# Kernel optimization log

Measured on AMD Instinct MI355X. Metric: run time of the kernel, lower is better.

## Reference

```python
import jax, jax.numpy as jnp
import numpy as np

N_NODES = 50000
N_EDGES = 800000
N_HIDDEN = 64
N_LAYER = 3
IN_DIM = 4


def setup_inputs() -> dict:
    key = jax.random.key(0)
    ks = jax.random.split(key, 10)
    x = jax.random.normal(ks[0], (N_NODES, IN_DIM), dtype=jnp.float32)
    edge_index = jax.random.randint(ks[1], (2, N_EDGES), 0, N_NODES, dtype=jnp.int64)
    # Glorot-style params matching pyg GCNConv (lin has no bias; conv adds bias after aggregation)
    def glorot(k, fan_in, fan_out):
        s = jnp.sqrt(6.0 / (fan_in + fan_out))
        return jax.random.uniform(k, (fan_in, fan_out), jnp.float32, -s, s)
    W_in = glorot(ks[2], IN_DIM, N_HIDDEN)
    b_in = jnp.zeros((N_HIDDEN,), jnp.float32)
    W_h = jnp.stack([glorot(jax.random.fold_in(ks[3], i), N_HIDDEN, N_HIDDEN) for i in range(N_LAYER)])
    b_h = jnp.zeros((N_LAYER, N_HIDDEN), jnp.float32)
    W_out = glorot(ks[4], N_HIDDEN, 1)
    b_out = jnp.zeros((1,), jnp.float32)
    return {"x": x, "edge_index": edge_index, "W_in": W_in, "b_in": b_in,
            "W_h": W_h, "b_h": b_h, "W_out": W_out, "b_out": b_out}


def _gcn_norm(edge_index, n_nodes):
    # add self-loops, compute symmetric norm D^{-1/2} (A+I) D^{-1/2}
    loop = jnp.arange(n_nodes, dtype=edge_index.dtype)
    src = jnp.concatenate([edge_index[0], loop])
    dst = jnp.concatenate([edge_index[1], loop])
    deg = jax.ops.segment_sum(jnp.ones_like(dst, dtype=jnp.float32), dst, num_segments=n_nodes)
    dinv = jax.lax.rsqrt(deg)  # deg >= 1 due to self-loops
    norm = dinv[src] * dinv[dst]
    return src, dst, norm


def _gcn_conv(x, W, b, src, dst, norm, n_nodes):
    h = x @ W                                   # [N, out]
    msg = h[src] * norm[:, None]                # gather + scale, [E+N, out]
    out = jax.ops.segment_sum(msg, dst, num_segments=n_nodes)  # scatter-add
    return out + b


def reference(x, edge_index, W_in, b_in, W_h, b_h, W_out, b_out):
    n = x.shape[0]
    src, dst, norm = _gcn_norm(edge_index, n)
    h = jax.nn.relu(_gcn_conv(x, W_in, b_in, src, dst, norm, n))
    for i in range(W_h.shape[0]):
        h = jax.nn.relu(_gcn_conv(h, W_h[i], b_h[i], src, dst, norm, n))
    return _gcn_conv(h, W_out, b_out, src, dst, norm, n)
```

## Files before the change

kernel.cpp:

```cpp
#include <hip/hip_runtime.h>
#include <hip/hip_bf16.h>


#define TPB 256
#define EPT 8
#define CHUNK (TPB * EPT)
typedef __hip_bfloat16 bf16;
#define B2F __bfloat162float

__global__ void k_zero_b(int* __restrict__ bktcnt, int* __restrict__ ticket) {
    bktcnt[threadIdx.x] = 0;
    if (threadIdx.x == 0) *ticket = 0;
}

__global__ __launch_bounds__(TPB) void k_bktcnt(
    const int* __restrict__ dst, int* __restrict__ bktcnt, int* __restrict__ ticket,
    int* __restrict__ bktbase, int* __restrict__ bcur, int E, int n) {
    __shared__ int h[256];
    __shared__ int lastFlag;
    int tid = threadIdx.x;
    h[tid] = 0;
    __syncthreads();
    int e0 = blockIdx.x * CHUNK;
#pragma unroll
    for (int u = 0; u < EPT; ++u) {
        int e = e0 + u * TPB + tid;
        if (e < E) {
            int d = dst[e];
            if ((unsigned)d < (unsigned)n) atomicAdd(&h[d >> 8], 1);
        }
    }
    __syncthreads();
    if (h[tid]) atomicAdd(&bktcnt[tid], h[tid]);
    __threadfence();
    __syncthreads();
    if (tid == 0) lastFlag = (atomicAdd(ticket, 1) == (int)gridDim.x - 1);
    __syncthreads();
    if (!lastFlag) return;
    int v = atomicAdd(&bktcnt[tid], 0);
    h[tid] = v;
    __syncthreads();
    for (int off = 1; off < 256; off <<= 1) {
        int u2 = (tid >= off) ? h[tid - off] : 0;
        __syncthreads();
        h[tid] += u2;
        __syncthreads();
    }
    int excl = h[tid] - v;
    bktbase[tid] = excl;
    bcur[tid] = excl;
    if (tid == 255) bktbase[256] = h[tid];
}

__global__ __launch_bounds__(TPB) void k_bin(
    const int* __restrict__ src, const int* __restrict__ dst,
    int* __restrict__ bcur, unsigned* __restrict__ staging, int E, int n) {
    __shared__ int hcnt[256];
    __shared__ int hbase[256];
    int tid = threadIdx.x;
    int e0 = blockIdx.x * CHUNK;
    hcnt[tid] = 0;
    __syncthreads();

    int eb[EPT];
    unsigned rec[EPT];
#pragma unroll
    for (int u = 0; u < EPT; ++u) {
        int e = e0 + u * TPB + tid;
        eb[u] = -1;
        if (e < E) {
            int d = dst[e], s = src[e];
            if ((unsigned)d < (unsigned)n && (unsigned)s < (unsigned)n) {
                eb[u] = d >> 8;
                rec[u] = (unsigned)s | ((unsigned)(d & 255) << 16);
                atomicAdd(&hcnt[eb[u]], 1);
            }
        }
    }
    __syncthreads();
    int c = hcnt[tid];
    hbase[tid] = (c > 0) ? atomicAdd(&bcur[tid], c) : 0;
    hcnt[tid] = 0;
    __syncthreads();
#pragma unroll
    for (int u = 0; u < EPT; ++u) {
        if (eb[u] >= 0) {
            int r = atomicAdd(&hcnt[eb[u]], 1);
            int pos = hbase[eb[u]] + r;
            if ((unsigned)pos < (unsigned)E) staging[pos] = rec[u];
        }
    }
}

__global__ __launch_bounds__(TPB) void k_unbin2(
    const unsigned* __restrict__ staging, const int* __restrict__ bktbase,
    const float* __restrict__ x, float4* __restrict__ xt,
    int* __restrict__ row_start, float* __restrict__ dinv,
    unsigned short* __restrict__ bucket, int E, int n) {
    __shared__ int cnt[256];
    __shared__ int scn[256];
    __shared__ int cur[256];
    int b = blockIdx.x, tid = threadIdx.x;
    int lo = bktbase[b], hi = bktbase[b + 1];
    lo = max(0, min(lo, E)); hi = max(lo, min(hi, E));

    cnt[tid] = 0;
    __syncthreads();
    for (int i = lo + tid; i < hi; i += TPB)
        atomicAdd(&cnt[(staging[i] >> 16) & 255], 1);
    __syncthreads();

    int v = cnt[tid];
    scn[tid] = v;
    __syncthreads();
    for (int off = 1; off < 256; off <<= 1) {
        int u = (tid >= off) ? scn[tid - off] : 0;
        __syncthreads();
        scn[tid] += u;
        __syncthreads();
    }
    int excl = scn[tid] - v;
    int base = min(lo + excl, E);
    cur[tid] = base;
    int d = (b << 8) + tid;
    if (d < n) {
        row_start[d] = base;
        float di = rsqrtf((float)v + 1.0f);
        dinv[d] = di;
        float4 xv = ((const float4*)x)[d];
        xv.x *= di; xv.y *= di; xv.z *= di; xv.w *= di;
        xt[d] = xv;
        if (d == n - 1) row_start[n] = min(base + v, E);
    }
    __syncthreads();

    for (int i = lo + tid; i < hi; i += TPB) {
        unsigned r = staging[i];
        int t = (r >> 16) & 255;
        int pos = atomicAdd(&cur[t], 1);
        if ((unsigned)pos < (unsigned)E) bucket[pos] = (unsigned short)(r & 0xffffu);
    }
}

__device__ __forceinline__ void acc_oct(float* a, uint4 w) {
    a[0] += __uint_as_float(w.x << 16);
    a[1] += __uint_as_float(w.x & 0xffff0000u);
    a[2] += __uint_as_float(w.y << 16);
    a[3] += __uint_as_float(w.y & 0xffff0000u);
    a[4] += __uint_as_float(w.z << 16);
    a[5] += __uint_as_float(w.z & 0xffff0000u);
    a[6] += __uint_as_float(w.w << 16);
    a[7] += __uint_as_float(w.w & 0xffff0000u);
}

__device__ __forceinline__ void agg_oct(const bf16* __restrict__ g,
                                        const unsigned short* __restrict__ bucket,
                                        int k0, int k1, int d, float* __restrict__ a,
                                        int lane, unsigned nm1, unsigned Em1) {
    int grp = lane >> 3, i = lane & 7;
#pragma unroll
    for (int m = 0; m < 8; ++m) a[m] = 0.f;
    if (grp == 0) {
        uint4 w = *(const uint4*)(g + (size_t)d * 64 + 8 * i);
        acc_oct(a, w);
    }
    for (int base = k0; base < k1; base += 64) {
        int cnt = min(64, k1 - base);
        int rec = bucket[min((unsigned)(base + lane), Em1)];
        int k = 0;
        for (; k + 16 <= cnt; k += 16) {
            unsigned s0 = min((unsigned)__shfl(rec, k + grp), nm1);
            unsigned s1 = min((unsigned)__shfl(rec, k + 8 + grp), nm1);
            uint4 w0 = *(const uint4*)(g + (size_t)s0 * 64 + 8 * i);
            uint4 w1 = *(const uint4*)(g + (size_t)s1 * 64 + 8 * i);
            acc_oct(a, w0);
            acc_oct(a, w1);
        }
        for (; k < cnt; k += 8) {
            int e = k + grp;
            unsigned s = min((unsigned)__shfl(rec, min(e, 63)), nm1);
            uint4 w = *(const uint4*)(g + (size_t)s * 64 + 8 * i);
            if (e < cnt) acc_oct(a, w);
        }
    }
}

__global__ __launch_bounds__(TPB, 4) void k_gconv1(
    const float4* __restrict__ xt, const float* __restrict__ dinv,
    const int* __restrict__ row_start, const unsigned short* __restrict__ bucket,
    const float* __restrict__ W_in, const float* __restrict__ b_in,
    const float* __restrict__ Wh0, bf16* __restrict__ gOut, int n, int E) {
    __shared__ float sAct[4][64];
    int tid = threadIdx.x;
    int r = tid >> 6, j = tid & 63;
    unsigned nm1 = (unsigned)(n - 1);

    float wreg[64];
#pragma unroll
    for (int k = 0; k < 64; ++k) wreg[k] = Wh0[k * 64 + j];
    float win0 = W_in[0 * 64 + j], win1 = W_in[1 * 64 + j];
    float win2 = W_in[2 * 64 + j], win3 = W_in[3 * 64 + j];
    float bj = b_in[j];

    int nw = gridDim.x * 4;
    for (int d = blockIdx.x * 4 + r; d < n; d += nw) {
        float dd = dinv[d];
        int k0 = row_start[d], k1 = row_start[d + 1];
        k1 = min(k1, E); k0 = max(min(k0, k1), 0);

        float4 v = make_float4(0.f, 0.f, 0.f, 0.f);
        if (j == 0) v = xt[d];
        for (int k = k0 + j; k < k1; k += 64) {
            unsigned s = min((unsigned)bucket[k], nm1);
            float4 t = xt[s];
            v.x += t.x; v.y += t.y; v.z += t.z; v.w += t.w;
        }
#pragma unroll
        for (int off = 1; off < 64; off <<= 1) {
            v.x += __shfl_xor(v.x, off);
            v.y += __shfl_xor(v.y, off);
            v.z += __shfl_xor(v.z, off);
            v.w += __shfl_xor(v.w, off);
        }
        float dot = fmaf(v.x, win0, fmaf(v.y, win1, fmaf(v.z, win2, v.w * win3)));
        float act = fmaxf(fmaf(dd, dot, bj), 0.f);
        sAct[r][j] = act;

        float acc0 = 0.f, acc1 = 0.f, acc2 = 0.f, acc3 = 0.f;
        const float4* ap = (const float4*)&sAct[r][0];
#pragma unroll
        for (int k4 = 0; k4 < 16; ++k4) {
            float4 av = ap[k4];
            acc0 = fmaf(av.x, wreg[4 * k4 + 0], acc0);
            acc1 = fmaf(av.y, wreg[4 * k4 + 1], acc1);
            acc2 = fmaf(av.z, wreg[4 * k4 + 2], acc2);
            acc3 = fmaf(av.w, wreg[4 * k4 + 3], acc3);
        }
        float acc = (acc0 + acc1) + (acc2 + acc3);
        gOut[(size_t)d * 64 + j] = __float2bfloat16(acc * dd);
    }
}

__global__ __launch_bounds__(TPB, 4) void k_gconv(
    const bf16* __restrict__ gIn, const float* __restrict__ dinv,
    const int* __restrict__ row_start, const unsigned short* __restrict__ bucket,
    const float* __restrict__ bias, const float* __restrict__ W,
    bf16* __restrict__ gOut, int n, int E) {
    __shared__ float sVp[4][8][68];
    int tid = threadIdx.x;
    int r = tid >> 6, j = tid & 63;
    int grp = j >> 3, i = j & 7;
    unsigned nm1 = (unsigned)(n - 1), Em1 = (unsigned)(E - 1);

    float wreg[64];
#pragma unroll
    for (int k = 0; k < 64; ++k) wreg[k] = W[k * 64 + j];
    float bj = bias[j];

    int nw = gridDim.x * 4;
    for (int d = blockIdx.x * 4 + r; d < n; d += nw) {
        float dd = dinv[d];
        int k0 = row_start[d], k1 = row_start[d + 1];
        k1 = min(k1, E); k0 = max(min(k0, k1), 0);

        float a[8];
        agg_oct(gIn, bucket, k0, k1, d, a, j, nm1, Em1);

        float4* prow = (float4*)&sVp[r][grp][8 * i];
        prow[0] = make_float4(a[0], a[1], a[2], a[3]);
        prow[1] = make_float4(a[4], a[5], a[6], a[7]);
        float full = 0.f;
#pragma unroll
        for (int g = 0; g < 8; ++g) full += sVp[r][g][j];

        float act = fmaxf(fmaf(dd, full, bj), 0.f);
        sVp[r][0][j] = act;

        float acc0 = 0.f, acc1 = 0.f, acc2 = 0.f, acc3 = 0.f;
#pragma unroll
        for (int k4 = 0; k4 < 16; ++k4) {
            float4 av = *(const float4*)&sVp[r][0][4 * k4];
            acc0 = fmaf(av.x, wreg[4 * k4 + 0], acc0);
            acc1 = fmaf(av.y, wreg[4 * k4 + 1], acc1);
            acc2 = fmaf(av.z, wreg[4 * k4 + 2], acc2);
            acc3 = fmaf(av.w, wreg[4 * k4 + 3], acc3);
        }
        float acc = (acc0 + acc1) + (acc2 + acc3);
        gOut[(size_t)d * 64 + j] = __float2bfloat16(acc * dd);
    }
}

__global__ __launch_bounds__(TPB) void k_gconv_z(
    const bf16* __restrict__ gIn, const float* __restrict__ dinv,
    const int* __restrict__ row_start, const unsigned short* __restrict__ bucket,
    const float* __restrict__ bias, const float* __restrict__ Wout,
    float* __restrict__ zg, int n, int E) {
    __shared__ float sVp[4][8][68];
    int tid = threadIdx.x;
    int r = tid >> 6, j = tid & 63;
    int grp = j >> 3, i = j & 7;
    int d = blockIdx.x * 4 + r;
    if (d >= n) return;
    float dd = dinv[d];
    int k0 = row_start[d], k1 = row_start[d + 1];
    k1 = min(k1, E); k0 = max(min(k0, k1), 0);

    float a[8];
    agg_oct(gIn, bucket, k0, k1, d, a, j, (unsigned)(n - 1), (unsigned)(E - 1));

    float4* prow = (float4*)&sVp[r][grp][8 * i];
    prow[0] = make_float4(a[0], a[1], a[2], a[3]);
    prow[1] = make_float4(a[4], a[5], a[6], a[7]);
    float full = 0.f;
#pragma unroll
    for (int g = 0; g < 8; ++g) full += sVp[r][g][j];

    float p = fmaxf(fmaf(dd, full, bias[j]), 0.f) * Wout[j];
#pragma unroll
    for (int off = 32; off > 0; off >>= 1) p += __shfl_down(p, off);
    if (j == 0) zg[d] = p * dd;
}

__global__ __launch_bounds__(TPB) void k_out(
    const float* __restrict__ zg, const float* __restrict__ dinv,
    const int* __restrict__ row_start, const unsigned short* __restrict__ bucket,
    const float* __restrict__ b_out, float* __restrict__ out, int n, int E) {
    int t = blockIdx.x * blockDim.x + threadIdx.x;
    int d = t >> 6, lane = t & 63;
    if (d >= n) return;
    int k0 = row_start[d], k1 = row_start[d + 1];
    k1 = min(k1, E); k0 = max(min(k0, k1), 0);
    unsigned nm1 = (unsigned)(n - 1);
    float v = 0.f;
    for (int k = k0 + lane; k < k1; k += 64) {
        unsigned s = min((unsigned)bucket[k], nm1);
        v += zg[s];
    }
#pragma unroll
    for (int off = 32; off > 0; off >>= 1) v += __shfl_down(v, off);
    if (lane == 0) out[d] = fmaf(zg[d] + v, dinv[d], b_out[0]);
}

extern "C" void kernel_launch(void* const* d_in, const int* in_sizes, int n_in,
                              void* d_out, int out_size, void* d_ws, size_t ws_size,
                              hipStream_t stream) {
    const float* x     = (const float*)d_in[0];
    const int*   ei    = (const int*)d_in[1];
    const float* W_in  = (const float*)d_in[2];
    const float* b_in  = (const float*)d_in[3];
    const float* W_h   = (const float*)d_in[4];
    const float* b_h   = (const float*)d_in[5];
    const float* W_out = (const float*)d_in[6];
    const float* b_out = (const float*)d_in[7];
    float* out = (float*)d_out;

    int N = in_sizes[0] / 4;
    int E = in_sizes[1] / 2;
    const int* src = ei;
    const int* dst = ei + E;

    char* ws = (char*)d_ws;
    bf16* gA               = (bf16*)ws;           ws += (size_t)N * 64 * 2;
    bf16* gB               = (bf16*)ws;           ws += (size_t)N * 64 * 2;
    float4* xt             = (float4*)ws;         ws += (size_t)N * 16;
    unsigned short* bucket = (unsigned short*)ws; ws += (size_t)E * 2;
    unsigned* staging      = (unsigned*)ws;       ws += (size_t)E * 4;
    int*  row_start        = (int*)ws;            ws += (size_t)(N + 1) * 4;
    float* dinv            = (float*)ws;          ws += (size_t)N * 4;
    float* zg              = (float*)ws;          ws += (size_t)N * 4;
    int*  bktcnt           = (int*)ws;            ws += 256 * 4;
    int*  ticket           = (int*)ws;            ws += 4;
    int*  bktbase          = (int*)ws;            ws += 257 * 4;
    int*  bcur             = (int*)ws;

    int B     = (N + 255) >> 8;
    int gN4   = (N + 3) / 4;
    int gPers = 1024;
    int gBin  = (E + CHUNK - 1) / CHUNK;

    k_zero_b<<<1, 256, 0, stream>>>(bktcnt, ticket);
    k_bktcnt<<<gBin, TPB, 0, stream>>>(dst, bktcnt, ticket, bktbase, bcur, E, N);
    k_bin<<<gBin, TPB, 0, stream>>>(src, dst, bcur, staging, E, N);
    k_unbin2<<<B, TPB, 0, stream>>>(staging, bktbase, x, xt, row_start, dinv, bucket, E, N);

    k_gconv1<<<gPers, TPB, 0, stream>>>(xt, dinv, row_start, bucket, W_in, b_in, W_h, gB, N, E);
    k_gconv<<<gPers, TPB, 0, stream>>>(gB, dinv, row_start, bucket, b_h, W_h + 4096, gA, N, E);
    k_gconv<<<gPers, TPB, 0, stream>>>(gA, dinv, row_start, bucket, b_h + 64, W_h + 8192, gB, N, E);
    k_gconv_z<<<gN4, TPB, 0, stream>>>(gB, dinv, row_start, bucket, b_h + 128, W_out, zg, N, E);
    k_out<<<gN4, TPB, 0, stream>>>(zg, dinv, row_start, bucket, b_out, out, N, E);
}
```

Measured before the change: 260.0 us.

## Replace two-level bucket sort CSR build with per-node degree count, scan, scatter

The CSR build changes from a 256-bucket two-pass binning with a staging buffer to a direct counting sort. It uses per-node global atomic degree counts, a two-level scan over node degrees, and an atomic scatter of source ids into per-node slots. This drops the staging buffer and the shared-memory sub-bucket pass, but adds one more launch and relies on global atomics to 50k counters twice. Neighbour order within a row becomes nondeterministic, which can change the float summation order and hurt gather locality.

After: 292.4 us. 12.5% more time.

```diff
diff --git a/kernel.cpp b/kernel.cpp
--- a/kernel.cpp
+++ b/kernel.cpp
@@ -8,139 +8,108 @@
 typedef __hip_bfloat16 bf16;
 #define B2F __bfloat162float
 
-__global__ void k_zero_b(int* __restrict__ bktcnt, int* __restrict__ ticket) {
-    bktcnt[threadIdx.x] = 0;
-    if (threadIdx.x == 0) *ticket = 0;
-}
-
-__global__ __launch_bounds__(TPB) void k_bktcnt(
-    const int* __restrict__ dst, int* __restrict__ bktcnt, int* __restrict__ ticket,
-    int* __restrict__ bktbase, int* __restrict__ bcur, int E, int n) {
-    __shared__ int h[256];
-    __shared__ int lastFlag;
-    int tid = threadIdx.x;
-    h[tid] = 0;
-    __syncthreads();
-    int e0 = blockIdx.x * CHUNK;
+
+__global__ void k_deg0(int* __restrict__ deg, int* __restrict__ ticket, int n) {
+    int t = blockIdx.x * blockDim.x + threadIdx.x;
+    if (t < n) deg[t] = 0;
+    if (t == 0) *ticket = 0;
+}
+
+__global__ __launch_bounds__(TPB) void k_deg(
+    const int* __restrict__ dst, int* __restrict__ deg, int E, int n) {
+    int e0 = blockIdx.x * CHUNK + threadIdx.x;
 #pragma unroll
     for (int u = 0; u < EPT; ++u) {
-        int e = e0 + u * TPB + tid;
+        int e = e0 + u * TPB;
         if (e < E) {
             int d = dst[e];
-            if ((unsigned)d < (unsigned)n) atomicAdd(&h[d >> 8], 1);
-        }
-    }
-    __syncthreads();
-    if (h[tid]) atomicAdd(&bktcnt[tid], h[tid]);
+            if ((unsigned)d < (unsigned)n) atomicAdd(&deg[d], 1);
+        }
+    }
+}
+
+__global__ __launch_bounds__(TPB) void k_scan1(
+    int* __restrict__ bsum, int* __restrict__ bbase, int* __restrict__ ticket,
+    const int* __restrict__ deg, int n) {
+    __shared__ int s[256];
+    __shared__ int lastFlag;
+    int b = blockIdx.x, tid = threadIdx.x;
+    int nb = gridDim.x;
+    int d = b * 256 + tid;
+    int v = (d < n) ? deg[d] : 0;
+    s[tid] = v;
+    __syncthreads();
+    for (int off = 128; off > 0; off >>= 1) {
+        if (tid < off) s[tid] += s[tid + off];
+        __syncthreads();
+    }
+    if (tid == 0) bsum[b] = s[0];
     __threadfence();
     __syncthreads();
-    if (tid == 0) lastFlag = (atomicAdd(ticket, 1) == (int)gridDim.x - 1);
+    if (tid == 0) lastFlag = (atomicAdd(ticket, 1) == nb - 1);
     __syncthreads();
     if (!lastFlag) return;
-    int v = atomicAdd(&bktcnt[tid], 0);
-    h[tid] = v;
+    int bv = (tid < nb) ? atomicAdd(&bsum[tid], 0) : 0;
+    s[tid] = bv;
     __syncthreads();
     for (int off = 1; off < 256; off <<= 1) {
-        int u2 = (tid >= off) ? h[tid - off] : 0;
-        __syncthreads();
-        h[tid] += u2;
-        __syncthreads();
-    }
-    int excl = h[tid] - v;
-    bktbase[tid] = excl;
-    bcur[tid] = excl;
-    if (tid == 255) bktbase[256] = h[tid];
-}
-
-__global__ __launch_bounds__(TPB) void k_bin(
-    const int* __restrict__ src, const int* __restrict__ dst,
-    int* __restrict__ bcur, unsigned* __restrict__ staging, int E, int n) {
-    __shared__ int hcnt[256];
-    __shared__ int hbase[256];
-    int tid = threadIdx.x;
-    int e0 = blockIdx.x * CHUNK;
-    hcnt[tid] = 0;
-    __syncthreads();
-
-    int eb[EPT];
-    unsigned rec[EPT];
-#pragma unroll
-    for (int u = 0; u < EPT; ++u) {
-        int e = e0 + u * TPB + tid;
-        eb[u] = -1;
-        if (e < E) {
-            int d = dst[e], s = src[e];
-            if ((unsigned)d < (unsigned)n && (unsigned)s < (unsigned)n) {
-                eb[u] = d >> 8;
-                rec[u] = (unsigned)s | ((unsigned)(d & 255) << 16);
-                atomicAdd(&hcnt[eb[u]], 1);
-            }
-        }
-    }
-    __syncthreads();
-    int c = hcnt[tid];
-    hbase[tid] = (c > 0) ? atomicAdd(&bcur[tid], c) : 0;
-    hcnt[tid] = 0;
-    __syncthreads();
-#pragma unroll
-    for (int u = 0; u < EPT; ++u) {
-        if (eb[u] >= 0) {
-            int r = atomicAdd(&hcnt[eb[u]], 1);
-            int pos = hbase[eb[u]] + r;
-            if ((unsigned)pos < (unsigned)E) staging[pos] = rec[u];
-        }
-    }
-}
-
-__global__ __launch_bounds__(TPB) void k_unbin2(
-    const unsigned* __restrict__ staging, const int* __restrict__ bktbase,
+        int u2 = (tid >= off) ? s[tid - off] : 0;
+        __syncthreads();
+        s[tid] += u2;
+        __syncthreads();
+    }
+    if (tid < nb) bbase[tid] = s[tid] - bv;
+    if (tid == nb - 1) bbase[nb] = s[tid];
+}
+
+__global__ __launch_bounds__(TPB) void k_scan2(
+    const int* __restrict__ deg, const int* __restrict__ bbase,
     const float* __restrict__ x, float4* __restrict__ xt,
     int* __restrict__ row_start, float* __restrict__ dinv,
-    unsigned short* __restrict__ bucket, int E, int n) {
-    __shared__ int cnt[256];
-    __shared__ int scn[256];
-    __shared__ int cur[256];
+    int* __restrict__ cur, int n) {
+    __shared__ int s[256];
     int b = blockIdx.x, tid = threadIdx.x;
-    int lo = bktbase[b], hi = bktbase[b + 1];
-    lo = max(0, min(lo, E)); hi = max(lo, min(hi, E));
-
-    cnt[tid] = 0;
-    __syncthreads();
-    for (int i = lo + tid; i < hi; i += TPB)
-        atomicAdd(&cnt[(staging[i] >> 16) & 255], 1);
-    __syncthreads();
-
-    int v = cnt[tid];
-    scn[tid] = v;
+    int d = b * 256 + tid;
+    int v = (d < n) ? deg[d] : 0;
+    s[tid] = v;
     __syncthreads();
     for (int off = 1; off < 256; off <<= 1) {
-        int u = (tid >= off) ? scn[tid - off] : 0;
-        __syncthreads();
-        scn[tid] += u;
-        __syncthreads();
-    }
-    int excl = scn[tid] - v;
-    int base = min(lo + excl, E);
-    cur[tid] = base;
-    int d = (b << 8) + tid;
+        int u2 = (tid >= off) ? s[tid - off] : 0;
+        __syncthreads();
+        s[tid] += u2;
+        __syncthreads();
+    }
+    int base = bbase[b] + (s[tid] - v);
     if (d < n) {
         row_start[d] = base;
+        cur[d] = base;
         float di = rsqrtf((float)v + 1.0f);
         dinv[d] = di;
         float4 xv = ((const float4*)x)[d];
         xv.x *= di; xv.y *= di; xv.z *= di; xv.w *= di;
         xt[d] = xv;
-        if (d == n - 1) row_start[n] = min(base + v, E);
-    }
-    __syncthreads();
-
-    for (int i = lo + tid; i < hi; i += TPB) {
-        unsigned r = staging[i];
-        int t = (r >> 16) & 255;
-        int pos = atomicAdd(&cur[t], 1);
-        if ((unsigned)pos < (unsigned)E) bucket[pos] = (unsigned short)(r & 0xffffu);
-    }
-}
+        if (d == n - 1) row_start[n] = base + v;
+    }
+}
+
+__global__ __launch_bounds__(TPB) void k_scat(
+    const int* __restrict__ src, const int* __restrict__ dst,
+    int* __restrict__ cur, unsigned short* __restrict__ bucket, int E, int n) {
+    int e0 = blockIdx.x * CHUNK + threadIdx.x;
+#pragma unroll
+    for (int u = 0; u < EPT; ++u) {
+        int e = e0 + u * TPB;
+        if (e < E) {
+            int d = dst[e], s = src[e];
+            if ((unsigned)d < (unsigned)n && (unsigned)s < (unsigned)n) {
+                int pos = atomicAdd(&cur[d], 1);
+                if ((unsigned)pos < (unsigned)E)
+                    bucket[pos] = (unsigned short)s;
+            }
+        }
+    }
+}
+
 
 __device__ __forceinline__ void acc_oct(float* a, uint4 w) {
     a[0] += __uint_as_float(w.x << 16);
@@ -364,24 +333,25 @@
     bf16* gB               = (bf16*)ws;           ws += (size_t)N * 64 * 2;
     float4* xt             = (float4*)ws;         ws += (size_t)N * 16;
     unsigned short* bucket = (unsigned short*)ws; ws += (size_t)E * 2;
-    unsigned* staging      = (unsigned*)ws;       ws += (size_t)E * 4;
     int*  row_start        = (int*)ws;            ws += (size_t)(N + 1) * 4;
     float* dinv            = (float*)ws;          ws += (size_t)N * 4;
     float* zg              = (float*)ws;          ws += (size_t)N * 4;
-    int*  bktcnt           = (int*)ws;            ws += 256 * 4;
-    int*  ticket           = (int*)ws;            ws += 4;
-    int*  bktbase          = (int*)ws;            ws += 257 * 4;
-    int*  bcur             = (int*)ws;
-
-    int B     = (N + 255) >> 8;
+    int*  deg              = (int*)ws;            ws += (size_t)N * 4;
+    int*  cur              = (int*)ws;            ws += (size_t)N * 4;
+    int*  bsum             = (int*)ws;            ws += 256 * 4;
+    int*  bbase            = (int*)ws;            ws += 257 * 4;
+    int*  ticket           = (int*)ws;
+
+    int nbN   = (N + 255) >> 8;
     int gN4   = (N + 3) / 4;
     int gPers = 1024;
-    int gBin  = (E + CHUNK - 1) / CHUNK;
-
-    k_zero_b<<<1, 256, 0, stream>>>(bktcnt, ticket);
-    k_bktcnt<<<gBin, TPB, 0, stream>>>(dst, bktcnt, ticket, bktbase, bcur, E, N);
-    k_bin<<<gBin, TPB, 0, stream>>>(src, dst, bcur, staging, E, N);
-    k_unbin2<<<B, TPB, 0, stream>>>(staging, bktbase, x, xt, row_start, dinv, bucket, E, N);
+    int gE    = (E + CHUNK - 1) / CHUNK;
+
+    k_deg0<<<nbN, TPB, 0, stream>>>(deg, ticket, N);
+    k_deg<<<gE, TPB, 0, stream>>>(dst, deg, E, N);
+    k_scan1<<<nbN, TPB, 0, stream>>>(bsum, bbase, ticket, deg, N);
+    k_scan2<<<nbN, TPB, 0, stream>>>(deg, bbase, x, xt, row_start, dinv, cur, N);
+    k_scat<<<gE, TPB, 0, stream>>>(src, dst, cur, bucket, E, N);
 
     k_gconv1<<<gPers, TPB, 0, stream>>>(xt, dinv, row_start, bucket, W_in, b_in, W_h, gB, N, E);
     k_gconv<<<gPers, TPB, 0, stream>>>(gB, dinv, row_start, bucket, b_h, W_h + 4096, gA, N, E);
```

## Stage hidden-layer weights in LDS and reduce partial sums with shuffles

Applied to the files above, without the earlier changes.

The hidden-layer conv kernel now loads its 64x64 weight matrix into shared memory once per block instead of holding a 64-float column per thread in registers. The cross-group reduction of the aggregated features moves from an LDS round trip to wave shuffles, and bias is read as float4. Lower register pressure lets launch bounds rise to 6 blocks per CU and the grid grow to 1536 persistent blocks, aiming for more latency hiding on the gather-bound aggregation. The trade is an LDS read for every FMA in the 64x64 matvec plus 16KB of LDS per block, which could limit occupancy or add bank pressure.

Result: slower. 390.3 us (+50.1%).

```diff
diff --git a/kernel.cpp b/kernel.cpp
--- a/kernel.cpp
+++ b/kernel.cpp
@@ -241,21 +241,27 @@
     }
 }
 
-__global__ __launch_bounds__(TPB, 4) void k_gconv(
+__global__ __launch_bounds__(TPB, 6) void k_gconv(
     const bf16* __restrict__ gIn, const float* __restrict__ dinv,
     const int* __restrict__ row_start, const unsigned short* __restrict__ bucket,
     const float* __restrict__ bias, const float* __restrict__ W,
     bf16* __restrict__ gOut, int n, int E) {
-    __shared__ float sVp[4][8][68];
+    __shared__ float sW[4096];
+    __shared__ float sAct[4][64];
     int tid = threadIdx.x;
+    {
+        const float4* W4 = (const float4*)W;
+        float4* sW4 = (float4*)sW;
+#pragma unroll
+        for (int t = 0; t < 4; ++t) sW4[tid + t * 256] = W4[tid + t * 256];
+    }
+    __syncthreads();
+
     int r = tid >> 6, j = tid & 63;
     int grp = j >> 3, i = j & 7;
     unsigned nm1 = (unsigned)(n - 1), Em1 = (unsigned)(E - 1);
-
-    float wreg[64];
-#pragma unroll
-    for (int k = 0; k < 64; ++k) wreg[k] = W[k * 64 + j];
-    float bj = bias[j];
+    const float4* b4 = (const float4*)bias;
+    float4 bA = b4[2 * i], bB = b4[2 * i + 1];
 
     int nw = gridDim.x * 4;
     for (int d = blockIdx.x * 4 + r; d < n; d += nw) {
@@ -266,24 +272,34 @@
         float a[8];
         agg_oct(gIn, bucket, k0, k1, d, a, j, nm1, Em1);
 
-        float4* prow = (float4*)&sVp[r][grp][8 * i];
-        prow[0] = make_float4(a[0], a[1], a[2], a[3]);
-        prow[1] = make_float4(a[4], a[5], a[6], a[7]);
-        float full = 0.f;
-#pragma unroll
-        for (int g = 0; g < 8; ++g) full += sVp[r][g][j];
-
-        float act = fmaxf(fmaf(dd, full, bj), 0.f);
-        sVp[r][0][j] = act;
-
+#pragma unroll
+        for (int m = 0; m < 8; ++m) {
+            a[m] += __shfl_xor(a[m], 8);
+            a[m] += __shfl_xor(a[m], 16);
+            a[m] += __shfl_xor(a[m], 32);
+        }
+        if (grp == 0) {
+            float4 r0, r1;
+            r0.x = fmaxf(fmaf(dd, a[0], bA.x), 0.f);
+            r0.y = fmaxf(fmaf(dd, a[1], bA.y), 0.f);
+            r0.z = fmaxf(fmaf(dd, a[2], bA.z), 0.f);
+            r0.w = fmaxf(fmaf(dd, a[3], bA.w), 0.f);
+            r1.x = fmaxf(fmaf(dd, a[4], bB.x), 0.f);
+            r1.y = fmaxf(fmaf(dd, a[5], bB.y), 0.f);
+            r1.z = fmaxf(fmaf(dd, a[6], bB.z), 0.f);
+            r1.w = fmaxf(fmaf(dd, a[7], bB.w), 0.f);
+            float4* arow = (float4*)&sAct[r][8 * i];
+            arow[0] = r0; arow[1] = r1;
+        }
         float acc0 = 0.f, acc1 = 0.f, acc2 = 0.f, acc3 = 0.f;
+        const float4* ap = (const float4*)&sAct[r][0];
 #pragma unroll
         for (int k4 = 0; k4 < 16; ++k4) {
-            float4 av = *(const float4*)&sVp[r][0][4 * k4];
-            acc0 = fmaf(av.x, wreg[4 * k4 + 0], acc0);
-            acc1 = fmaf(av.y, wreg[4 * k4 + 1], acc1);
-            acc2 = fmaf(av.z, wreg[4 * k4 + 2], acc2);
-            acc3 = fmaf(av.w, wreg[4 * k4 + 3], acc3);
+            float4 av = ap[k4];
+            acc0 = fmaf(av.x, sW[(4 * k4 + 0) * 64 + j], acc0);
+            acc1 = fmaf(av.y, sW[(4 * k4 + 1) * 64 + j], acc1);
+            acc2 = fmaf(av.z, sW[(4 * k4 + 2) * 64 + j], acc2);
+            acc3 = fmaf(av.w, sW[(4 * k4 + 3) * 64 + j], acc3);
         }
         float acc = (acc0 + acc1) + (acc2 + acc3);
         gOut[(size_t)d * 64 + j] = __float2bfloat16(acc * dd);
@@ -376,6 +392,7 @@
     int B     = (N + 255) >> 8;
     int gN4   = (N + 3) / 4;
     int gPers = 1024;
+    int gP6   = 1536;
     int gBin  = (E + CHUNK - 1) / CHUNK;
 
     k_zero_b<<<1, 256, 0, stream>>>(bktcnt, ticket);
@@ -384,8 +401,8 @@
     k_unbin2<<<B, TPB, 0, stream>>>(staging, bktbase, x, xt, row_start, dinv, bucket, E, N);
 
     k_gconv1<<<gPers, TPB, 0, stream>>>(xt, dinv, row_start, bucket, W_in, b_in, W_h, gB, N, E);
-    k_gconv<<<gPers, TPB, 0, stream>>>(gB, dinv, row_start, bucket, b_h, W_h + 4096, gA, N, E);
-    k_gconv<<<gPers, TPB, 0, stream>>>(gA, dinv, row_start, bucket, b_h + 64, W_h + 8192, gB, N, E);
+    k_gconv<<<gP6, TPB, 0, stream>>>(gB, dinv, row_start, bucket, b_h, W_h + 4096, gA, N, E);
+    k_gconv<<<gP6, TPB, 0, stream>>>(gA, dinv, row_start, bucket, b_h + 64, W_h + 8192, gB, N, E);
     k_gconv_z<<<gN4, TPB, 0, stream>>>(gB, dinv, row_start, bucket, b_h + 128, W_out, zg, N, E);
     k_out<<<gN4, TPB, 0, stream>>>(zg, dinv, row_start, bucket, b_out, out, N, E);
 }
```
